# Performance work log

Measured on AMD Instinct MI355X. Metric: run time of the kernel, lower is better.

## Reference

```python
import jax, jax.numpy as jnp
import numpy as np

N_NODES = 100000
N_EDGES = 1600000
IN_FEATS = 64
NUM_CLASSES = 64


def setup_inputs() -> dict:
    key = jax.random.key(0)
    k1, k2, k3, k4, k5, k6 = jax.random.split(key, 6)
    in_feat = jax.random.normal(k1, (N_NODES, IN_FEATS), dtype=jnp.float32)
    src = jax.random.randint(k2, (N_EDGES,), 0, N_NODES, dtype=jnp.int32)
    dst = jax.random.randint(k3, (N_EDGES,), 0, N_NODES, dtype=jnp.int32)
    scale = 1.0 / np.sqrt(IN_FEATS)
    W_self = jax.random.normal(k4, (IN_FEATS, NUM_CLASSES), dtype=jnp.float32) * scale
    W_neigh = jax.random.normal(k5, (IN_FEATS, NUM_CLASSES), dtype=jnp.float32) * scale
    bias = jax.random.normal(k6, (NUM_CLASSES,), dtype=jnp.float32) * 0.01
    return {"in_feat": in_feat, "src": src, "dst": dst,
            "W_self": W_self, "W_neigh": W_neigh, "bias": bias}


def reference(in_feat, src, dst, W_self, W_neigh, bias):
    # SAGEConv with 'mean' aggregator (DGL semantics):
    #   h_neigh[v] = mean over incoming edges (u->v) of in_feat[u]; 0 if no in-edges
    #   out = fc_self(x) + fc_neigh(h_neigh) + bias, then sigmoid
    n = in_feat.shape[0]
    msg = in_feat[src]                                            # [E, F] gather
    agg = jax.ops.segment_sum(msg, dst, num_segments=n)           # [N, F]
    deg = jax.ops.segment_sum(jnp.ones((src.shape[0],), jnp.float32), dst,
                              num_segments=n)                     # [N]
    h_neigh = agg / jnp.maximum(deg, 1.0)[:, None]                # mean, 0 for isolated
    out = in_feat @ W_self + h_neigh @ W_neigh + bias
    return jax.nn.sigmoid(out)
```

## Files before the change

kernel.cpp:

```cpp
#include <hip/hip_runtime.h>


constexpr int NN = 100000;
constexpr int NE = 1600000;
constexpr int F  = 64;
constexpr int RB = 256;
constexpr int NB = (NN + RB - 1) / RB;
constexpr int CH = 8192;
constexpr int PB = (NE + CH - 1) / CH;

typedef short bf16x8 __attribute__((ext_vector_type(8)));
typedef float f32x4  __attribute__((ext_vector_type(4)));
typedef unsigned short u16;
typedef u16 u16x8 __attribute__((ext_vector_type(8)));

__device__ __forceinline__ u16 f2bf(float f) {
    unsigned u = __float_as_uint(f);
    unsigned r = (u + 0x7FFF + ((u >> 16) & 1)) >> 16;
    return (u16)r;
}

__global__ __launch_bounds__(256) void k_cvt8(const float* __restrict__ x,
                                              unsigned char* __restrict__ x8) {
    const int i = (blockIdx.x * 256 + threadIdx.x) * 8;
    if (i >= NN * F) return;
    float4 a = *(const float4*)&x[i];
    float4 b = *(const float4*)&x[i + 4];
    int lo = 0, hi = 0;
    lo = __builtin_amdgcn_cvt_pk_fp8_f32(a.x, a.y, lo, false);
    lo = __builtin_amdgcn_cvt_pk_fp8_f32(a.z, a.w, lo, true);
    hi = __builtin_amdgcn_cvt_pk_fp8_f32(b.x, b.y, hi, false);
    hi = __builtin_amdgcn_cvt_pk_fp8_f32(b.z, b.w, hi, true);
    *(int2*)&x8[i] = make_int2(lo, hi);
}

__global__ __launch_bounds__(256) void k_hist(const int* __restrict__ dst,
                                              int* __restrict__ gcount) {
    __shared__ int h[NB];
    for (int i = threadIdx.x; i < NB; i += 256) h[i] = 0;
    __syncthreads();
    const int b0  = blockIdx.x * CH;
    const int end = min(b0 + CH, NE);
    for (int i = b0 + threadIdx.x * 4; i < end; i += 1024) {
        int4 d = *(const int4*)&dst[i];
        atomicAdd(&h[d.x >> 8], 1);
        atomicAdd(&h[d.y >> 8], 1);
        atomicAdd(&h[d.z >> 8], 1);
        atomicAdd(&h[d.w >> 8], 1);
    }
    __syncthreads();
    for (int i = threadIdx.x; i < NB; i += 256)
        if (h[i]) atomicAdd(&gcount[i], h[i]);
}

__global__ __launch_bounds__(512) void k_scan(const int* __restrict__ gcount,
                                              int* __restrict__ basep,
                                              int* __restrict__ cursor) {
    __shared__ int tmp[512];
    const int t = threadIdx.x;
    int val = (t < NB) ? gcount[t] : 0;
    tmp[t] = val;
    __syncthreads();
    int s = val;
    for (int o = 1; o < 512; o <<= 1) {
        int add = (t >= o) ? tmp[t - o] : 0;
        __syncthreads();
        s += add;
        tmp[t] = s;
        __syncthreads();
    }
    if (t < NB) {
        basep[t]  = s - val;
        cursor[t] = s - val;
    }
}

__global__ __launch_bounds__(512) void k_part(const int* __restrict__ src,
                                              const int* __restrict__ dst,
                                              int* __restrict__ cursor,
                                              unsigned* __restrict__ packed) {
    __shared__ unsigned stage[CH];
    __shared__ unsigned short bkt[CH];
    __shared__ int hist[NB], lscan[NB], lcur[NB], gpos[NB];
    __shared__ int tmp[512];

    const int t   = threadIdx.x;
    const int b0  = blockIdx.x * CH;
    const int cnt = min(CH, NE - b0);

    for (int i = t; i < NB; i += 512) hist[i] = 0;
    __syncthreads();

    int4 sv[4], dv[4];
#pragma unroll
    for (int j = 0; j < 4; ++j) {
        const int idx = j * 2048 + t * 4;
        if (idx < cnt) {
            sv[j] = *(const int4*)&src[b0 + idx];
            dv[j] = *(const int4*)&dst[b0 + idx];
            atomicAdd(&hist[dv[j].x >> 8], 1);
            atomicAdd(&hist[dv[j].y >> 8], 1);
            atomicAdd(&hist[dv[j].z >> 8], 1);
            atomicAdd(&hist[dv[j].w >> 8], 1);
        }
    }
    __syncthreads();

    int val = (t < NB) ? hist[t] : 0;
    tmp[t] = val;
    __syncthreads();
    int s = val;
    for (int o = 1; o < 512; o <<= 1) {
        int add = (t >= o) ? tmp[t - o] : 0;
        __syncthreads();
        s += add;
        tmp[t] = s;
        __syncthreads();
    }
    if (t < NB) {
        lscan[t] = s - val;
        lcur[t]  = s - val;
        gpos[t]  = val ? atomicAdd(&cursor[t], val) : 0;
    }
    __syncthreads();

#pragma unroll
    for (int j = 0; j < 4; ++j) {
        const int idx = j * 2048 + t * 4;
        if (idx < cnt) {
            const int ss[4] = {sv[j].x, sv[j].y, sv[j].z, sv[j].w};
            const int dd[4] = {dv[j].x, dv[j].y, dv[j].z, dv[j].w};
#pragma unroll
            for (int q = 0; q < 4; ++q) {
                const int b = dd[q] >> 8;
                const int p = atomicAdd(&lcur[b], 1);
                stage[p] = ((unsigned)(dd[q] & 255) << 17) | (unsigned)ss[q];
                bkt[p]   = (unsigned short)b;
            }
        }
    }
    __syncthreads();

    for (int i = t; i < cnt; i += 512) {
        const int b = bkt[i];
        packed[gpos[b] + (i - lscan[b])] = stage[i];
    }
}

__global__ __launch_bounds__(256) void k_bsort(const unsigned* __restrict__ packed,
                                               const int* __restrict__ basep,
                                               int* __restrict__ ssrc,
                                               int* __restrict__ off,
                                               int* __restrict__ degi) {
    __shared__ int hist[RB];
    __shared__ int cur[RB];
    const int b = blockIdx.x;
    const int t = threadIdx.x;
    const int e0 = basep[b];
    const int e1 = (b == NB - 1) ? NE : basep[b + 1];
    const int m  = e1 - e0;

    hist[t] = 0;
    __syncthreads();
    for (int i = t; i < m; i += 256)
        atomicAdd(&hist[packed[e0 + i] >> 17], 1);
    __syncthreads();

    const int val = hist[t];
    cur[t] = val;
    __syncthreads();
    int s = val;
    for (int o = 1; o < 256; o <<= 1) {
        int add = (t >= o) ? cur[t - o] : 0;
        __syncthreads();
        s += add;
        cur[t] = s;
        __syncthreads();
    }
    const int ex = s - val;
    const int v = b * RB + t;
    if (v < NN) {
        off[v]  = e0 + ex;
        degi[v] = val;
    }
    cur[t] = ex;
    __syncthreads();

    for (int i = t; i < m; i += 256) {
        const unsigned p = packed[e0 + i];
        const int pos = atomicAdd(&cur[p >> 17], 1);
        ssrc[e0 + pos] = (int)(p & 0x1FFFFu);
    }
}

__device__ __forceinline__ void acc8(f32x4& lo, f32x4& hi, int2 q) {
    lo[0] += __builtin_amdgcn_cvt_f32_fp8(q.x, 0);
    lo[1] += __builtin_amdgcn_cvt_f32_fp8(q.x, 1);
    lo[2] += __builtin_amdgcn_cvt_f32_fp8(q.x, 2);
    lo[3] += __builtin_amdgcn_cvt_f32_fp8(q.x, 3);
    hi[0] += __builtin_amdgcn_cvt_f32_fp8(q.y, 0);
    hi[1] += __builtin_amdgcn_cvt_f32_fp8(q.y, 1);
    hi[2] += __builtin_amdgcn_cvt_f32_fp8(q.y, 2);
    hi[3] += __builtin_amdgcn_cvt_f32_fp8(q.y, 3);
}

__global__ __launch_bounds__(512) void k_fused(
    const unsigned char* __restrict__ x8, const float* __restrict__ x,
    const int* __restrict__ off, const int* __restrict__ degi,
    const int* __restrict__ ssrc,
    const float* __restrict__ Ws, const float* __restrict__ Wn,
    const float* __restrict__ bias, float* __restrict__ out)
{
    __shared__ u16 At[64 * 128];

    const int base = blockIdx.x * 64;
    const int nv   = min(64, NN - base);
    const int t    = threadIdx.x;
    const int r    = t >> 3;
    const int cg   = t & 7;

    if (r < nv) {
        const int v  = base + r;
        const int e0 = off[v];
        const int dg = degi[v];
        f32x4 alo = {0.f, 0.f, 0.f, 0.f}, ahi = alo;
        int e = 0;
        for (; e + 4 <= dg; e += 4) {
            const int s0 = ssrc[e0 + e + 0];
            const int s1 = ssrc[e0 + e + 1];
            const int s2 = ssrc[e0 + e + 2];
            const int s3 = ssrc[e0 + e + 3];
            int2 q0 = *(const int2*)&x8[(size_t)s0 * F + cg * 8];
            int2 q1 = *(const int2*)&x8[(size_t)s1 * F + cg * 8];
            int2 q2 = *(const int2*)&x8[(size_t)s2 * F + cg * 8];
            int2 q3 = *(const int2*)&x8[(size_t)s3 * F + cg * 8];
            acc8(alo, ahi, q0);
            acc8(alo, ahi, q1);
            acc8(alo, ahi, q2);
            acc8(alo, ahi, q3);
        }
        for (; e < dg; ++e) {
            int2 q = *(const int2*)&x8[(size_t)ssrc[e0 + e] * F + cg * 8];
            acc8(alo, ahi, q);
        }
        const float inv = 1.0f / fmaxf((float)dg, 1.0f);

        u16x8 hb;
        hb[0] = f2bf(alo[0] * inv); hb[1] = f2bf(alo[1] * inv);
        hb[2] = f2bf(alo[2] * inv); hb[3] = f2bf(alo[3] * inv);
        hb[4] = f2bf(ahi[0] * inv); hb[5] = f2bf(ahi[1] * inv);
        hb[6] = f2bf(ahi[2] * inv); hb[7] = f2bf(ahi[3] * inv);
        const int bh = (8 + cg) ^ (r & 15);
        *(u16x8*)&At[r * 128 + bh * 8] = hb;

        float4 xa = *(const float4*)&x[(size_t)v * F + cg * 8];
        float4 xc = *(const float4*)&x[(size_t)v * F + cg * 8 + 4];
        u16x8 xv;
        xv[0] = f2bf(xa.x); xv[1] = f2bf(xa.y); xv[2] = f2bf(xa.z); xv[3] = f2bf(xa.w);
        xv[4] = f2bf(xc.x); xv[5] = f2bf(xc.y); xv[6] = f2bf(xc.z); xv[7] = f2bf(xc.w);
        const int bx = cg ^ (r & 15);
        *(u16x8*)&At[r * 128 + bx * 8] = xv;
    }
    __syncthreads();

    const int w    = t >> 6;
    const int lane = t & 63;
    const int tr   = w >> 1;
    if (tr * 16 >= nv) return;
    const int nh   = w & 1;
    const int r16  = lane & 15;
    const int kg   = lane >> 4;

    bf16x8 bf[4][2];
#pragma unroll
    for (int t4 = 0; t4 < 4; ++t4)
#pragma unroll
        for (int uu = 0; uu < 2; ++uu)
#pragma unroll
            for (int j = 0; j < 8; ++j) {
                const int kk = t4 * 32 + kg * 8 + j;
                const int n  = (nh * 2 + uu) * 16 + r16;
                const float wv = (kk < 64) ? Ws[kk * 64 + n] : Wn[(kk - 64) * 64 + n];
                bf[t4][uu][j] = (short)f2bf(wv);
            }
    const float b0 = bias[(nh * 2 + 0) * 16 + r16];
    const float b1 = bias[(nh * 2 + 1) * 16 + r16];

    const int row = tr * 16 + r16;
    bf16x8 a[4];
#pragma unroll
    for (int t4 = 0; t4 < 4; ++t4) {
        const int blk = (t4 * 4 + kg) ^ (row & 15);
        a[t4] = *(const bf16x8*)&At[row * 128 + blk * 8];
    }

    f32x4 c0 = {0.f, 0.f, 0.f, 0.f}, c1 = c0;
    c0 = __builtin_amdgcn_mfma_f32_16x16x32_bf16(a[0], bf[0][0], c0, 0, 0, 0);
    c0 = __builtin_amdgcn_mfma_f32_16x16x32_bf16(a[1], bf[1][0], c0, 0, 0, 0);
    c0 = __builtin_amdgcn_mfma_f32_16x16x32_bf16(a[2], bf[2][0], c0, 0, 0, 0);
    c0 = __builtin_amdgcn_mfma_f32_16x16x32_bf16(a[3], bf[3][0], c0, 0, 0, 0);
    c1 = __builtin_amdgcn_mfma_f32_16x16x32_bf16(a[0], bf[0][1], c1, 0, 0, 0);
    c1 = __builtin_amdgcn_mfma_f32_16x16x32_bf16(a[1], bf[1][1], c1, 0, 0, 0);
    c1 = __builtin_amdgcn_mfma_f32_16x16x32_bf16(a[2], bf[2][1], c1, 0, 0, 0);
    c1 = __builtin_amdgcn_mfma_f32_16x16x32_bf16(a[3], bf[3][1], c1, 0, 0, 0);

    float* orow = out + (size_t)(base + tr * 16) * 64;
#pragma unroll
    for (int rr = 0; rr < 4; ++rr) {
        const int ro = (kg * 4 + rr) * 64;
        orow[ro + (nh * 2 + 0) * 16 + r16] = 1.0f / (1.0f + __expf(-(c0[rr] + b0)));
        orow[ro + (nh * 2 + 1) * 16 + r16] = 1.0f / (1.0f + __expf(-(c1[rr] + b1)));
    }
}

extern "C" void kernel_launch(void* const* d_in, const int* in_sizes, int n_in,
                              void* d_out, int out_size, void* d_ws, size_t ws_size,
                              hipStream_t stream) {
    const float* x    = (const float*)d_in[0];
    const int*   src  = (const int*)d_in[1];
    const int*   dst  = (const int*)d_in[2];
    const float* Ws   = (const float*)d_in[3];
    const float* Wn   = (const float*)d_in[4];
    const float* bias = (const float*)d_in[5];
    float* out = (float*)d_out;

    unsigned char* x8 = (unsigned char*)d_ws;
    int* gcount = (int*)(x8 + (size_t)NN * F);
    int* basep  = gcount + NB;
    int* cursor = basep + NB;
    int* off    = cursor + NB;
    int* degi   = off + NN;
    unsigned* packed = (unsigned*)(degi + NN);
    int* ssrc   = (int*)(packed + NE);

    hipMemsetAsync(gcount, 0, (size_t)NB * sizeof(int), stream);

    k_cvt8 <<<(NN * F / 8 + 255) / 256, 256, 0, stream>>>(x, x8);
    k_hist <<<PB, 256, 0, stream>>>(dst, gcount);
    k_scan <<<1, 512, 0, stream>>>(gcount, basep, cursor);
    k_part <<<PB, 512, 0, stream>>>(src, dst, cursor, packed);
    k_bsort<<<NB, 256, 0, stream>>>(packed, basep, ssrc, off, degi);

    k_fused<<<(NN + 63) / 64, 512, 0, stream>>>(x8, x, off, degi, ssrc,
                                                Ws, Wn, bias, out);
}
```

Baseline: 95.04 us.

## Fold per-node bucket sort into the fused kernel and precompute bf16 operands

Removes the separate k_bsort pass. Each fused block now rescans its 256-node bucket of packed edges, keeps only its 64-node quarter, builds a local histogram, scan and sorted staging of source indices in LDS, and gathers from there. The prep kernel also writes a bf16 copy of x and a pre-transposed bf16 weight matrix, so the fused kernel loads ready MFMA operands instead of converting per block. FP8 accumulation switches to packed conversion builtins. The trade-off is that four blocks redundantly read each bucket twice, and more than CAP edges per 64 nodes would be silently dropped.

```diff
diff --git a/kernel.cpp b/kernel.cpp
--- a/kernel.cpp
+++ b/kernel.cpp
@@ -8,9 +8,11 @@
 constexpr int NB = (NN + RB - 1) / RB;
 constexpr int CH = 8192;
 constexpr int PB = (NE + CH - 1) / CH;
+constexpr int CAP = 2048;
 
 typedef short bf16x8 __attribute__((ext_vector_type(8)));
 typedef float f32x4  __attribute__((ext_vector_type(4)));
+typedef float f32x2  __attribute__((ext_vector_type(2)));
 typedef unsigned short u16;
 typedef u16 u16x8 __attribute__((ext_vector_type(8)));
 
@@ -20,18 +22,40 @@
     return (u16)r;
 }
 
-__global__ __launch_bounds__(256) void k_cvt8(const float* __restrict__ x,
-                                              unsigned char* __restrict__ x8) {
-    const int i = (blockIdx.x * 256 + threadIdx.x) * 8;
-    if (i >= NN * F) return;
-    float4 a = *(const float4*)&x[i];
-    float4 b = *(const float4*)&x[i + 4];
-    int lo = 0, hi = 0;
-    lo = __builtin_amdgcn_cvt_pk_fp8_f32(a.x, a.y, lo, false);
-    lo = __builtin_amdgcn_cvt_pk_fp8_f32(a.z, a.w, lo, true);
-    hi = __builtin_amdgcn_cvt_pk_fp8_f32(b.x, b.y, hi, false);
-    hi = __builtin_amdgcn_cvt_pk_fp8_f32(b.z, b.w, hi, true);
-    *(int2*)&x8[i] = make_int2(lo, hi);
+__global__ __launch_bounds__(256) void k_prep(const float* __restrict__ x,
+                                              const float* __restrict__ Ws,
+                                              const float* __restrict__ Wn,
+                                              unsigned char* __restrict__ x8,
+                                              u16* __restrict__ xb,
+                                              u16* __restrict__ Bt) {
+    const int i = blockIdx.x * 256 + threadIdx.x;
+    if (i < NN * F / 8) {
+        const int o = i * 8;
+        float4 a = *(const float4*)&x[o];
+        float4 b = *(const float4*)&x[o + 4];
+        int lo = 0, hi = 0;
+        lo = __builtin_amdgcn_cvt_pk_fp8_f32(a.x, a.y, lo, false);
+        lo = __builtin_amdgcn_cvt_pk_fp8_f32(a.z, a.w, lo, true);
+        hi = __builtin_amdgcn_cvt_pk_fp8_f32(b.x, b.y, hi, false);
+        hi = __builtin_amdgcn_cvt_pk_fp8_f32(b.z, b.w, hi, true);
+        *(int2*)&x8[o] = make_int2(lo, hi);
+        u16x8 r;
+        r[0] = f2bf(a.x); r[1] = f2bf(a.y); r[2] = f2bf(a.z); r[3] = f2bf(a.w);
+        r[4] = f2bf(b.x); r[5] = f2bf(b.y); r[6] = f2bf(b.z); r[7] = f2bf(b.w);
+        *(u16x8*)&xb[o] = r;
+    } else if (i < NN * F / 8 + 1024) {
+        const int j  = i - NN * F / 8;
+        const int n  = j >> 4;
+        const int kb = (j & 15) * 8;
+        u16x8 r;
+#pragma unroll
+        for (int jj = 0; jj < 8; ++jj) {
+            const int kk = kb + jj;
+            const float w = (kk < 64) ? Ws[kk * 64 + n] : Wn[(kk - 64) * 64 + n];
+            r[jj] = f2bf(w);
+        }
+        *(u16x8*)&Bt[n * 128 + kb] = r;
+    }
 }
 
 __global__ __launch_bounds__(256) void k_hist(const int* __restrict__ dst,
@@ -147,119 +171,116 @@
     }
 }
 
-__global__ __launch_bounds__(256) void k_bsort(const unsigned* __restrict__ packed,
-                                               const int* __restrict__ basep,
-                                               int* __restrict__ ssrc,
-                                               int* __restrict__ off,
-                                               int* __restrict__ degi) {
-    __shared__ int hist[RB];
-    __shared__ int cur[RB];
-    const int b = blockIdx.x;
-    const int t = threadIdx.x;
-    const int e0 = basep[b];
-    const int e1 = (b == NB - 1) ? NE : basep[b + 1];
-    const int m  = e1 - e0;
-
-    hist[t] = 0;
-    __syncthreads();
-    for (int i = t; i < m; i += 256)
-        atomicAdd(&hist[packed[e0 + i] >> 17], 1);
-    __syncthreads();
-
-    const int val = hist[t];
-    cur[t] = val;
-    __syncthreads();
-    int s = val;
-    for (int o = 1; o < 256; o <<= 1) {
-        int add = (t >= o) ? cur[t - o] : 0;
-        __syncthreads();
-        s += add;
-        cur[t] = s;
-        __syncthreads();
-    }
-    const int ex = s - val;
-    const int v = b * RB + t;
-    if (v < NN) {
-        off[v]  = e0 + ex;
-        degi[v] = val;
-    }
-    cur[t] = ex;
-    __syncthreads();
-
-    for (int i = t; i < m; i += 256) {
-        const unsigned p = packed[e0 + i];
-        const int pos = atomicAdd(&cur[p >> 17], 1);
-        ssrc[e0 + pos] = (int)(p & 0x1FFFFu);
-    }
-}
-
-__device__ __forceinline__ void acc8(f32x4& lo, f32x4& hi, int2 q) {
-    lo[0] += __builtin_amdgcn_cvt_f32_fp8(q.x, 0);
-    lo[1] += __builtin_amdgcn_cvt_f32_fp8(q.x, 1);
-    lo[2] += __builtin_amdgcn_cvt_f32_fp8(q.x, 2);
-    lo[3] += __builtin_amdgcn_cvt_f32_fp8(q.x, 3);
-    hi[0] += __builtin_amdgcn_cvt_f32_fp8(q.y, 0);
-    hi[1] += __builtin_amdgcn_cvt_f32_fp8(q.y, 1);
-    hi[2] += __builtin_amdgcn_cvt_f32_fp8(q.y, 2);
-    hi[3] += __builtin_amdgcn_cvt_f32_fp8(q.y, 3);
+__device__ __forceinline__ void acc8pk(f32x2& a0, f32x2& a1, f32x2& a2, f32x2& a3,
+                                       int2 qq) {
+#if __has_builtin(__builtin_amdgcn_cvt_pk_f32_fp8)
+    a0 += __builtin_amdgcn_cvt_pk_f32_fp8(qq.x, false);
+    a1 += __builtin_amdgcn_cvt_pk_f32_fp8(qq.x, true);
+    a2 += __builtin_amdgcn_cvt_pk_f32_fp8(qq.y, false);
+    a3 += __builtin_amdgcn_cvt_pk_f32_fp8(qq.y, true);
+#else
+    a0[0] += __builtin_amdgcn_cvt_f32_fp8(qq.x, 0);
+    a0[1] += __builtin_amdgcn_cvt_f32_fp8(qq.x, 1);
+    a1[0] += __builtin_amdgcn_cvt_f32_fp8(qq.x, 2);
+    a1[1] += __builtin_amdgcn_cvt_f32_fp8(qq.x, 3);
+    a2[0] += __builtin_amdgcn_cvt_f32_fp8(qq.y, 0);
+    a2[1] += __builtin_amdgcn_cvt_f32_fp8(qq.y, 1);
+    a3[0] += __builtin_amdgcn_cvt_f32_fp8(qq.y, 2);
+    a3[1] += __builtin_amdgcn_cvt_f32_fp8(qq.y, 3);
+#endif
 }
 
 __global__ __launch_bounds__(512) void k_fused(
-    const unsigned char* __restrict__ x8, const float* __restrict__ x,
-    const int* __restrict__ off, const int* __restrict__ degi,
-    const int* __restrict__ ssrc,
-    const float* __restrict__ Ws, const float* __restrict__ Wn,
-    const float* __restrict__ bias, float* __restrict__ out)
+    const unsigned char* __restrict__ x8, const u16* __restrict__ xb,
+    const unsigned* __restrict__ packed, const int* __restrict__ basep,
+    const u16* __restrict__ Bt, const float* __restrict__ bias,
+    float* __restrict__ out)
 {
     __shared__ u16 At[64 * 128];
-
-    const int base = blockIdx.x * 64;
+    __shared__ unsigned stage[CAP];
+    __shared__ int hist[64], cur[64], exar[64];
+
+    const int blk  = blockIdx.x;
+    const int base = blk * 64;
+    const int bu   = blk >> 2;
+    const int qq   = blk & 3;
+    const int t    = threadIdx.x;
     const int nv   = min(64, NN - base);
-    const int t    = threadIdx.x;
-    const int r    = t >> 3;
-    const int cg   = t & 7;
-
+
+    const int e0 = basep[bu];
+    const int e1 = (bu == NB - 1) ? NE : basep[bu + 1];
+    const int m  = e1 - e0;
+
+    if (t < 64) hist[t] = 0;
+    __syncthreads();
+
+    for (int i = t; i < m; i += 512) {
+        const unsigned p  = packed[e0 + i];
+        const unsigned dl = p >> 17;
+        if ((int)(dl >> 6) == qq) atomicAdd(&hist[dl & 63], 1);
+    }
+    __syncthreads();
+
+    if (t < 64) {
+        const int val = hist[t];
+        int s = val;
+#pragma unroll
+        for (int o = 1; o < 64; o <<= 1) {
+            const int nsh = __shfl_up(s, o);
+            if (t >= o) s += nsh;
+        }
+        cur[t]  = s - val;
+        exar[t] = s - val;
+    }
+    __syncthreads();
+
+    for (int i = t; i < m; i += 512) {
+        const unsigned p  = packed[e0 + i];
+        const unsigned dl = p >> 17;
+        if ((int)(dl >> 6) == qq) {
+            const int pos = atomicAdd(&cur[dl & 63], 1);
+            if (pos < CAP) stage[pos] = p & 0x1FFFFu;
+        }
+    }
+    __syncthreads();
+
+    const int r  = t >> 3;
+    const int cg = t & 7;
     if (r < nv) {
-        const int v  = base + r;
-        const int e0 = off[v];
-        const int dg = degi[v];
-        f32x4 alo = {0.f, 0.f, 0.f, 0.f}, ahi = alo;
+        const int dg = hist[r];
+        const int s0 = exar[r];
+        f32x2 a0 = {0.f, 0.f}, a1 = a0, a2 = a0, a3 = a0;
         int e = 0;
         for (; e + 4 <= dg; e += 4) {
-            const int s0 = ssrc[e0 + e + 0];
-            const int s1 = ssrc[e0 + e + 1];
-            const int s2 = ssrc[e0 + e + 2];
-            const int s3 = ssrc[e0 + e + 3];
-            int2 q0 = *(const int2*)&x8[(size_t)s0 * F + cg * 8];
-            int2 q1 = *(const int2*)&x8[(size_t)s1 * F + cg * 8];
-            int2 q2 = *(const int2*)&x8[(size_t)s2 * F + cg * 8];
-            int2 q3 = *(const int2*)&x8[(size_t)s3 * F + cg * 8];
-            acc8(alo, ahi, q0);
-            acc8(alo, ahi, q1);
-            acc8(alo, ahi, q2);
-            acc8(alo, ahi, q3);
+            const int i0 = stage[s0 + e + 0];
+            const int i1 = stage[s0 + e + 1];
+            const int i2 = stage[s0 + e + 2];
+            const int i3 = stage[s0 + e + 3];
+            int2 q0 = *(const int2*)&x8[(size_t)i0 * F + cg * 8];
+            int2 q1 = *(const int2*)&x8[(size_t)i1 * F + cg * 8];
+            int2 q2 = *(const int2*)&x8[(size_t)i2 * F + cg * 8];
+            int2 q3 = *(const int2*)&x8[(size_t)i3 * F + cg * 8];
+            acc8pk(a0, a1, a2, a3, q0);
+            acc8pk(a0, a1, a2, a3, q1);
+            acc8pk(a0, a1, a2, a3, q2);
+            acc8pk(a0, a1, a2, a3, q3);
         }
         for (; e < dg; ++e) {
-            int2 q = *(const int2*)&x8[(size_t)ssrc[e0 + e] * F + cg * 8];
-            acc8(alo, ahi, q);
+            int2 q = *(const int2*)&x8[(size_t)stage[s0 + e] * F + cg * 8];
+            acc8pk(a0, a1, a2, a3, q);
         }
         const float inv = 1.0f / fmaxf((float)dg, 1.0f);
 
         u16x8 hb;
-        hb[0] = f2bf(alo[0] * inv); hb[1] = f2bf(alo[1] * inv);
-        hb[2] = f2bf(alo[2] * inv); hb[3] = f2bf(alo[3] * inv);
-        hb[4] = f2bf(ahi[0] * inv); hb[5] = f2bf(ahi[1] * inv);
-        hb[6] = f2bf(ahi[2] * inv); hb[7] = f2bf(ahi[3] * inv);
+        hb[0] = f2bf(a0[0] * inv); hb[1] = f2bf(a0[1] * inv);
+        hb[2] = f2bf(a1[0] * inv); hb[3] = f2bf(a1[1] * inv);
+        hb[4] = f2bf(a2[0] * inv); hb[5] = f2bf(a2[1] * inv);
+        hb[6] = f2bf(a3[0] * inv); hb[7] = f2bf(a3[1] * inv);
         const int bh = (8 + cg) ^ (r & 15);
         *(u16x8*)&At[r * 128 + bh * 8] = hb;
 
-        float4 xa = *(const float4*)&x[(size_t)v * F + cg * 8];
-        float4 xc = *(const float4*)&x[(size_t)v * F + cg * 8 + 4];
-        u16x8 xv;
-        xv[0] = f2bf(xa.x); xv[1] = f2bf(xa.y); xv[2] = f2bf(xa.z); xv[3] = f2bf(xa.w);
-        xv[4] = f2bf(xc.x); xv[5] = f2bf(xc.y); xv[6] = f2bf(xc.z); xv[7] = f2bf(xc.w);
         const int bx = cg ^ (r & 15);
-        *(u16x8*)&At[r * 128 + bx * 8] = xv;
+        *(u16x8*)&At[r * 128 + bx * 8] = *(const u16x8*)&xb[(size_t)(base + r) * F + cg * 8];
     }
     __syncthreads();
 
@@ -275,14 +296,10 @@
 #pragma unroll
     for (int t4 = 0; t4 < 4; ++t4)
 #pragma unroll
-        for (int uu = 0; uu < 2; ++uu)
-#pragma unroll
-            for (int j = 0; j < 8; ++j) {
-                const int kk = t4 * 32 + kg * 8 + j;
-                const int n  = (nh * 2 + uu) * 16 + r16;
-                const float wv = (kk < 64) ? Ws[kk * 64 + n] : Wn[(kk - 64) * 64 + n];
-                bf[t4][uu][j] = (short)f2bf(wv);
-            }
+        for (int uu = 0; uu < 2; ++uu) {
+            const int n = (nh * 2 + uu) * 16 + r16;
+            bf[t4][uu] = *(const bf16x8*)&Bt[n * 128 + t4 * 32 + kg * 8];
+        }
     const float b0 = bias[(nh * 2 + 0) * 16 + r16];
     const float b1 = bias[(nh * 2 + 1) * 16 + r16];
 
@@ -290,8 +307,8 @@
     bf16x8 a[4];
 #pragma unroll
     for (int t4 = 0; t4 < 4; ++t4) {
-        const int blk = (t4 * 4 + kg) ^ (row & 15);
-        a[t4] = *(const bf16x8*)&At[row * 128 + blk * 8];
+        const int blk16 = (t4 * 4 + kg) ^ (row & 15);
+        a[t4] = *(const bf16x8*)&At[row * 128 + blk16 * 8];
     }
 
     f32x4 c0 = {0.f, 0.f, 0.f, 0.f}, c1 = c0;
@@ -325,22 +342,19 @@
     float* out = (float*)d_out;
 
     unsigned char* x8 = (unsigned char*)d_ws;
-    int* gcount = (int*)(x8 + (size_t)NN * F);
+    u16* xb     = (u16*)(x8 + (size_t)NN * F);
+    u16* Bt     = xb + (size_t)NN * F;
+    int* gcount = (int*)(Bt + 64 * 128);
     int* basep  = gcount + NB;
     int* cursor = basep + NB;
-    int* off    = cursor + NB;
-    int* degi   = off + NN;
-    unsigned* packed = (unsigned*)(degi + NN);
-    int* ssrc   = (int*)(packed + NE);
+    unsigned* packed = (unsigned*)(cursor + NB);
 
     hipMemsetAsync(gcount, 0, (size_t)NB * sizeof(int), stream);
 
-    k_cvt8 <<<(NN * F / 8 + 255) / 256, 256, 0, stream>>>(x, x8);
+    k_prep <<<(NN * F / 8 + 1024 + 255) / 256, 256, 0, stream>>>(x, Ws, Wn, x8, xb, Bt);
     k_hist <<<PB, 256, 0, stream>>>(dst, gcount);
     k_scan <<<1, 512, 0, stream>>>(gcount, basep, cursor);
     k_part <<<PB, 512, 0, stream>>>(src, dst, cursor, packed);
-    k_bsort<<<NB, 256, 0, stream>>>(packed, basep, ssrc, off, degi);
-
-    k_fused<<<(NN + 63) / 64, 512, 0, stream>>>(x8, x, off, degi, ssrc,
-                                                Ws, Wn, bias, out);
-}
+
+    k_fused<<<(NN + 63) / 64, 512, 0, stream>>>(x8, xb, packed, basep, Bt, bias, out);
+}
```

New measurement: 87.74 us. 1.08x faster.
